# Optimization experiments

Measured on AMD Instinct MI355X. Metric: run time of the kernel, lower is better.

The kernel has to match this reference:

```python
import jax, jax.numpy as jnp
import numpy as np

B, H, S, D = 2, 16, 2048, 64
MASK_P = 0.1  # sparse random mask; avoids all-heads-masked NaN under softmax(dim=1)


def setup_inputs() -> dict:
    key = jax.random.key(0)
    kq, kk, kv, km = jax.random.split(key, 4)
    Q = jax.random.normal(kq, (B, H, S, D), dtype=jnp.float32)
    K = jax.random.normal(kk, (B, H, S, D), dtype=jnp.float32)
    V = jax.random.normal(kv, (B, H, S, D), dtype=jnp.float32)
    mask_bool = jax.random.uniform(km, (B, H, S, S)) < MASK_P
    return {"Q": Q, "K": K, "V": V, "mask_bool": mask_bool, "head_dim": D}


def reference(Q, K, V, mask_bool, head_dim):
    scale = jnp.sqrt(jnp.asarray(head_dim, dtype=Q.dtype))
    # scores: [B, H, Sq, Sk]
    scores = jnp.einsum("bhqd,bhkd->bhqk", Q, K) / scale
    scores = jnp.where(mask_bool, -jnp.inf, scores)
    # NOTE: source uses torch.softmax(..., dim=1) -> normalize over HEADS axis.
    attention_weight = jax.nn.softmax(scores, axis=1)
    # dropout module treated as identity (eval mode)
    context = jnp.einsum("bhqk,bhkd->bhqd", attention_weight, V)
    # transpose(1, 2) -> [B, Sq, H, D]
    return jnp.transpose(context, (0, 2, 1, 3))
```

## Files before the change

### kernel.cpp

```cpp
#include <hip/hip_runtime.h>
#include <stdint.h>
#include <math.h>

#define BB 2
#define HH 16
#define SS 2048
#define DD 64
#define QE  ((size_t)BB * HH * SS * DD)
#define PME ((size_t)BB * SS * SS)

#define WROW 36

typedef __attribute__((ext_vector_type(8))) short short8;
typedef __attribute__((ext_vector_type(4))) float float4v;

__device__ __forceinline__ float bflo(unsigned int u){ return __uint_as_float(u << 16); }
__device__ __forceinline__ float bfhi(unsigned int u){ return __uint_as_float(u & 0xffff0000u); }
__device__ __forceinline__ unsigned short f2bf(float f){
  unsigned int u = __float_as_uint(f);
  u += 0x7fffu + ((u >> 16) & 1u);
  return (unsigned short)(u >> 16);
}
__device__ __forceinline__ unsigned int pk2(float lo, float hi){
  return ((unsigned int)f2bf(hi) << 16) | (unsigned int)f2bf(lo);
}

__global__ void detect_mask_mode(const unsigned int* __restrict__ mw, int* __restrict__ mode_out){
  __shared__ int a32, af, a64;
  const int t = threadIdx.x;
  if (t == 0){ a32 = 1; af = 1; a64 = 1; }
  __syncthreads();
  int ok32 = 1, okf = 1, ok64 = 1;
  for (int idx = t; idx < 4096; idx += 256){
    const unsigned int w = mw[idx];
    if (w > 1u) ok32 = 0;
    if (w != 0u && w != 0x3F800000u) okf = 0;
    if ((idx & 1) ? (w != 0u) : (w > 1u)) ok64 = 0;
  }
  if (!ok32) atomicAnd(&a32, 0);
  if (!okf)  atomicAnd(&af, 0);
  if (!ok64) atomicAnd(&a64, 0);
  __syncthreads();
  if (t == 0){
    int mode;
    if (a64)      mode = 3;
    else if (a32) mode = 0;
    else if (af)  mode = 2;
    else          mode = 1;
    *mode_out = mode;
  }
}

__global__ __launch_bounds__(256) void pack_mask_kernel(
    const void* __restrict__ mask, const int* __restrict__ modep,
    unsigned short* __restrict__ pm)
{
  const int mode = *modep;
  const size_t tid  = (size_t)blockIdx.x * 256 + threadIdx.x;
  const size_t base = tid * 8;
  const size_t bq   = base >> 11;
  const int    k0   = (int)(base & (SS - 1));
  const size_t b    = bq >> 11;
  const size_t q    = bq & (SS - 1);

  unsigned short outv[8] = {0,0,0,0,0,0,0,0};

  if (mode == 0 || mode == 2){
    const unsigned int* p = (const unsigned int*)mask;
    #pragma unroll
    for (int h = 0; h < HH; ++h){
      const size_t e = ((b * HH + h) * SS + q) * SS + k0;
      const uint4 a = *(const uint4*)(p + e);
      const uint4 c = *(const uint4*)(p + e + 4);
      const unsigned short bit = (unsigned short)(1u << h);
      if (a.x) outv[0] |= bit;  if (a.y) outv[1] |= bit;
      if (a.z) outv[2] |= bit;  if (a.w) outv[3] |= bit;
      if (c.x) outv[4] |= bit;  if (c.y) outv[5] |= bit;
      if (c.z) outv[6] |= bit;  if (c.w) outv[7] |= bit;
    }
  } else if (mode == 1){
    const unsigned char* p = (const unsigned char*)mask;
    #pragma unroll
    for (int h = 0; h < HH; ++h){
      const size_t e = ((b * HH + h) * SS + q) * SS + k0;
      uint2 a = *(const uint2*)(p + e);
      const unsigned short bit = (unsigned short)(1u << h);
      #pragma unroll
      for (int j = 0; j < 4; ++j){
        if ((a.x >> (8*j)) & 0xffu) outv[j]     |= bit;
        if ((a.y >> (8*j)) & 0xffu) outv[4 + j] |= bit;
      }
    }
  } else {
    const unsigned int* p = (const unsigned int*)mask;
    #pragma unroll
    for (int h = 0; h < HH; ++h){
      const size_t e = (((b * HH + h) * SS + q) * SS + k0) * 2;
      const unsigned short bit = (unsigned short)(1u << h);
      #pragma unroll
      for (int j = 0; j < 4; ++j){
        const uint4 a = *(const uint4*)(p + e + j * 4);
        if (a.x) outv[j * 2]     |= bit;
        if (a.z) outv[j * 2 + 1] |= bit;
      }
    }
  }

  uint4 w;
  w.x = (unsigned int)outv[0] | ((unsigned int)outv[1] << 16);
  w.y = (unsigned int)outv[2] | ((unsigned int)outv[3] << 16);
  w.z = (unsigned int)outv[4] | ((unsigned int)outv[5] << 16);
  w.w = (unsigned int)outv[6] | ((unsigned int)outv[7] << 16);
  *(uint4*)(pm + base) = w;
}

__global__ void conv_bf16_kernel(const float* __restrict__ src, unsigned short* __restrict__ dst, float scale){
  const size_t i = ((size_t)blockIdx.x * 256 + threadIdx.x) * 8;
  const float4 a = *(const float4*)(src + i);
  const float4 b = *(const float4*)(src + i + 4);
  uint4 o;
  o.x = pk2(a.x * scale, a.y * scale);
  o.y = pk2(a.z * scale, a.w * scale);
  o.z = pk2(b.x * scale, b.y * scale);
  o.w = pk2(b.z * scale, b.w * scale);
  *(uint4*)(dst + i) = o;
}

__global__ void transp_v_kernel(const float* __restrict__ V, unsigned short* __restrict__ Vt){
  __shared__ unsigned short tile[64][66];
  const int t  = threadIdx.x;
  const int kt = blockIdx.x & 31;
  const int bh = blockIdx.x >> 5;
  {
    const int kr = t >> 2, dc = (t & 3) * 16;
    const float* src = V + ((size_t)bh * SS + (size_t)(kt * 64 + kr)) * DD + dc;
    #pragma unroll
    for (int c = 0; c < 4; ++c){
      const float4 v = *(const float4*)(src + c * 4);
      tile[kr][dc + c * 4 + 0] = f2bf(v.x);
      tile[kr][dc + c * 4 + 1] = f2bf(v.y);
      tile[kr][dc + c * 4 + 2] = f2bf(v.z);
      tile[kr][dc + c * 4 + 3] = f2bf(v.w);
    }
  }
  __syncthreads();
  {
    const int dr = t >> 2, kc = (t & 3) * 16;
    unsigned short* dst = Vt + ((size_t)bh * DD + dr) * SS + kt * 64 + kc;
    unsigned int w[8];
    #pragma unroll
    for (int p = 0; p < 8; ++p){
      w[p] = (unsigned int)tile[kc + 2*p][dr] | ((unsigned int)tile[kc + 2*p + 1][dr] << 16);
    }
    uint4 o0 = { w[0], w[1], w[2], w[3] };
    uint4 o1 = { w[4], w[5], w[6], w[7] };
    *(uint4*)(dst)     = o0;
    *(uint4*)(dst + 8) = o1;
  }
}

__global__ __launch_bounds__(128, 2) void attn_main_kernel(
    const unsigned short* __restrict__ Qb, const unsigned short* __restrict__ Kb,
    const unsigned short* __restrict__ Vt, const unsigned short* __restrict__ pm,
    float* __restrict__ out)
{
  __shared__ unsigned int Wp[2][8 * 16 * WROW];

  const int t = threadIdx.x;
  const int wave = t >> 6, lane = t & 63, quad = lane >> 4, l16 = lane & 15;

  const int L  = blockIdx.x;
  const int kc = L & 3;
  const int b  = (L >> 2) & 1;
  const int q0 = (L >> 3) << 4;

  float4v O[8][4];
  #pragma unroll
  for (int i = 0; i < 8; ++i)
    #pragma unroll
    for (int j = 0; j < 4; ++j) O[i][j] = (float4v){0.f, 0.f, 0.f, 0.f};

  const unsigned short* qbase = Qb + ((size_t)(b * HH) * SS + (size_t)(q0 + l16)) * DD + quad * 8;
  const unsigned short* kbas0 = Kb + ((size_t)(b * HH) * SS + (size_t)(kc * 512 + wave * 16 + l16)) * DD + quad * 8;
  const unsigned short* pmrow = pm + ((size_t)b * SS + (size_t)(q0 + quad * 4)) * SS + (size_t)(kc * 512 + wave * 16 + l16);

  unsigned int m16[4];
  #pragma unroll
  for (int r = 0; r < 4; ++r) m16[r] = (unsigned int)pmrow[(size_t)r * SS];

  #pragma unroll 1
  for (int ks = 0; ks < 16; ++ks){
    const int k0 = kc * 512 + ks * 32;

    unsigned int sp[HH][2];
    const unsigned short* kbase = kbas0 + (size_t)ks * 32 * DD;

    #pragma unroll
    for (int ch = 0; ch < 8; ++ch){
      short8 qa0[2], qa1[2], kb0[2], kb1[2];
      #pragma unroll
      for (int j = 0; j < 2; ++j){
        const int h = ch * 2 + j;
        const unsigned short* qp = qbase + (size_t)h * (SS * DD);
        const unsigned short* kp = kbase + (size_t)h * (SS * DD);
        qa0[j] = *(const short8*)(qp);
        qa1[j] = *(const short8*)(qp + 32);
        kb0[j] = *(const short8*)(kp);
        kb1[j] = *(const short8*)(kp + 32);
      }
      #pragma unroll
      for (int j = 0; j < 2; ++j){
        const int h = ch * 2 + j;
        float4v c = (float4v){0.f, 0.f, 0.f, 0.f};
        c = __builtin_amdgcn_mfma_f32_16x16x32_bf16(qa0[j], kb0[j], c, 0, 0, 0);
        c = __builtin_amdgcn_mfma_f32_16x16x32_bf16(qa1[j], kb1[j], c, 0, 0, 0);
        #pragma unroll
        for (int r = 0; r < 4; ++r) if ((m16[r] >> h) & 1u) c[r] = -INFINITY;
        sp[h][0] = pk2(c[0], c[1]);
        sp[h][1] = pk2(c[2], c[3]);
      }
    }

    if (ks < 15){
      #pragma unroll
      for (int r = 0; r < 4; ++r) m16[r] = (unsigned int)pmrow[(size_t)r * SS + (size_t)(ks + 1) * 32];
    }

    unsigned int* Wc = &Wp[ks & 1][0];
    const int kdx = wave * 16 + l16;
    #pragma unroll
    for (int r = 0; r < 4; ++r){
      const int row = quad * 4 + r;
      float sv[HH];
      float m = -INFINITY;
      #pragma unroll
      for (int h = 0; h < HH; ++h){
        const unsigned int u = sp[h][r >> 1];
        const float f = (r & 1) ? bfhi(u) : bflo(u);
        sv[h] = f;
        m = fmaxf(m, f);
      }
      float sum = 0.f;
      #pragma unroll
      for (int h = 0; h < HH; ++h){
        const float e = (sv[h] != -INFINITY) ? __expf(sv[h] - m) : 0.f;
        sv[h] = e;
        sum += e;
      }
      const float rinv = (sum > 0.f) ? (1.0f / sum) : 0.f;
      #pragma unroll
      for (int hp = 0; hp < 8; ++hp){
        Wc[hp * (16 * WROW) + row * WROW + kdx] = pk2(sv[2 * hp] * rinv, sv[2 * hp + 1] * rinv);
      }
    }
    __syncthreads();

    #pragma unroll
    for (int hp2 = 0; hp2 < 4; ++hp2){
      const int hp = wave * 4 + hp2;
      const unsigned int* wb = &Wc[hp * (16 * WROW) + l16 * WROW + quad * 8];
      const uint4 da = *(const uint4*)(wb);
      const uint4 db = *(const uint4*)(wb + 4);
      const unsigned int d0 = da.x, d1 = da.y, d2 = da.z, d3 = da.w;
      const unsigned int d4 = db.x, d5 = db.y, d6 = db.z, d7 = db.w;
      uint4 ue, uo;
      ue.x = (d0 & 0xffffu) | (d1 << 16);
      ue.y = (d2 & 0xffffu) | (d3 << 16);
      ue.z = (d4 & 0xffffu) | (d5 << 16);
      ue.w = (d6 & 0xffffu) | (d7 << 16);
      uo.x = (d0 >> 16) | (d1 & 0xffff0000u);
      uo.y = (d2 >> 16) | (d3 & 0xffff0000u);
      uo.z = (d4 >> 16) | (d5 & 0xffff0000u);
      uo.w = (d6 >> 16) | (d7 & 0xffff0000u);
      const short8 ae = __builtin_bit_cast(short8, ue);
      const short8 ao = __builtin_bit_cast(short8, uo);

      const unsigned short* ve = Vt + ((size_t)(b * HH + 2 * hp) * DD + l16) * SS + k0 + quad * 8;
      const unsigned short* vo = ve + (size_t)SS * DD;
      #pragma unroll
      for (int dt = 0; dt < 4; ++dt){
        const short8 bve = *(const short8*)(ve + (size_t)dt * 16 * SS);
        const short8 bvo = *(const short8*)(vo + (size_t)dt * 16 * SS);
        O[hp2 * 2 + 0][dt] = __builtin_amdgcn_mfma_f32_16x16x32_bf16(ae, bve, O[hp2 * 2 + 0][dt], 0, 0, 0);
        O[hp2 * 2 + 1][dt] = __builtin_amdgcn_mfma_f32_16x16x32_bf16(ao, bvo, O[hp2 * 2 + 1][dt], 0, 0, 0);
      }
    }
  }

  #pragma unroll
  for (int hh = 0; hh < 8; ++hh){
    const int h = wave * 8 + hh;
    #pragma unroll
    for (int dt = 0; dt < 4; ++dt){
      #pragma unroll
      for (int r = 0; r < 4; ++r){
        float* op = out + (((size_t)b * SS + (size_t)(q0 + quad * 4 + r)) * HH + h) * DD + dt * 16 + l16;
        unsafeAtomicAdd(op, O[hh][dt][r]);
      }
    }
  }
}

extern "C" void kernel_launch(void* const* d_in, const int* in_sizes, int n_in,
                              void* d_out, int out_size, void* d_ws, size_t ws_size,
                              hipStream_t stream)
{
  const float* Q = (const float*)d_in[0];
  const float* K = (const float*)d_in[1];
  const float* V = (const float*)d_in[2];
  const void* mask = d_in[3];

  uintptr_t base = (uintptr_t)d_ws;
  int* mode_ptr       = (int*)base;
  unsigned short* Qb  = (unsigned short*)(base + 64);
  unsigned short* Kb  = Qb + QE;
  unsigned short* Vt  = Kb + QE;
  unsigned short* pmp = Vt + QE;

  detect_mask_mode<<<1, 256, 0, stream>>>((const unsigned int*)mask, mode_ptr);
  pack_mask_kernel<<<(int)(PME / (256 * 8)), 256, 0, stream>>>(mask, mode_ptr, pmp);
  conv_bf16_kernel<<<2048, 256, 0, stream>>>(Q, Qb, 0.125f);
  conv_bf16_kernel<<<2048, 256, 0, stream>>>(K, Kb, 1.0f);
  transp_v_kernel<<<BB * HH * (SS / 64), 256, 0, stream>>>(V, Vt);
  hipMemsetAsync(d_out, 0, (size_t)out_size * sizeof(float), stream);

  attn_main_kernel<<<1024, 128, 0, stream>>>(Qb, Kb, Vt, pmp, (float*)d_out);
}
```

Before: 1.124 ms.

## Split attention kernel into producer score waves and consumer PV waves

The main kernel becomes warp-specialized. Two waves compute QK scores, the mask and the head-axis softmax into double-buffered shared memory, and two waves run the PV MFMAs with register-prefetched V tiles. Q is staged once into shared memory and reused across key steps. The key split per block goes from 4 chunks to 2, with 256-thread blocks and half as many blocks, which cuts the atomic adds on the output. The producer and consumer loops sync through matching __syncthreads calls, and this relies on equal iteration counts in both branches.

```diff
diff --git a/kernel.cpp b/kernel.cpp
--- a/kernel.cpp
+++ b/kernel.cpp
@@ -159,143 +159,175 @@
   }
 }
 
-__global__ __launch_bounds__(128, 2) void attn_main_kernel(
+__global__ __launch_bounds__(256, 2) void attn_main_kernel(
     const unsigned short* __restrict__ Qb, const unsigned short* __restrict__ Kb,
     const unsigned short* __restrict__ Vt, const unsigned short* __restrict__ pm,
     float* __restrict__ out)
 {
-  __shared__ unsigned int Wp[2][8 * 16 * WROW];
+  __shared__ unsigned short Qf[HH * 2 * 512];
+  __shared__ unsigned int  Wp[2][8 * 16 * WROW];
 
   const int t = threadIdx.x;
   const int wave = t >> 6, lane = t & 63, quad = lane >> 4, l16 = lane & 15;
 
   const int L  = blockIdx.x;
-  const int kc = L & 3;
-  const int b  = (L >> 2) & 1;
-  const int q0 = (L >> 3) << 4;
-
-  float4v O[8][4];
+  const int b  = (L >> 1) & 1;
+  const int kc = (L >> 2) & 1;
+  const int q0 = (((L >> 3) << 1) | (L & 1)) * 16;
+
   #pragma unroll
-  for (int i = 0; i < 8; ++i)
-    #pragma unroll
-    for (int j = 0; j < 4; ++j) O[i][j] = (float4v){0.f, 0.f, 0.f, 0.f};
-
-  const unsigned short* qbase = Qb + ((size_t)(b * HH) * SS + (size_t)(q0 + l16)) * DD + quad * 8;
-  const unsigned short* kbas0 = Kb + ((size_t)(b * HH) * SS + (size_t)(kc * 512 + wave * 16 + l16)) * DD + quad * 8;
-  const unsigned short* pmrow = pm + ((size_t)b * SS + (size_t)(q0 + quad * 4)) * SS + (size_t)(kc * 512 + wave * 16 + l16);
-
-  unsigned int m16[4];
-  #pragma unroll
-  for (int r = 0; r < 4; ++r) m16[r] = (unsigned int)pmrow[(size_t)r * SS];
-
-  #pragma unroll 1
-  for (int ks = 0; ks < 16; ++ks){
-    const int k0 = kc * 512 + ks * 32;
-
-    unsigned int sp[HH][2];
-    const unsigned short* kbase = kbas0 + (size_t)ks * 32 * DD;
-
-    #pragma unroll
-    for (int ch = 0; ch < 8; ++ch){
-      short8 qa0[2], qa1[2], kb0[2], kb1[2];
-      #pragma unroll
-      for (int j = 0; j < 2; ++j){
-        const int h = ch * 2 + j;
-        const unsigned short* qp = qbase + (size_t)h * (SS * DD);
-        const unsigned short* kp = kbase + (size_t)h * (SS * DD);
-        qa0[j] = *(const short8*)(qp);
-        qa1[j] = *(const short8*)(qp + 32);
-        kb0[j] = *(const short8*)(kp);
-        kb1[j] = *(const short8*)(kp + 32);
-      }
-      #pragma unroll
-      for (int j = 0; j < 2; ++j){
-        const int h = ch * 2 + j;
-        float4v c = (float4v){0.f, 0.f, 0.f, 0.f};
-        c = __builtin_amdgcn_mfma_f32_16x16x32_bf16(qa0[j], kb0[j], c, 0, 0, 0);
-        c = __builtin_amdgcn_mfma_f32_16x16x32_bf16(qa1[j], kb1[j], c, 0, 0, 0);
-        #pragma unroll
-        for (int r = 0; r < 4; ++r) if ((m16[r] >> h) & 1u) c[r] = -INFINITY;
-        sp[h][0] = pk2(c[0], c[1]);
-        sp[h][1] = pk2(c[2], c[3]);
-      }
-    }
-
-    if (ks < 15){
-      #pragma unroll
-      for (int r = 0; r < 4; ++r) m16[r] = (unsigned int)pmrow[(size_t)r * SS + (size_t)(ks + 1) * 32];
-    }
-
-    unsigned int* Wc = &Wp[ks & 1][0];
-    const int kdx = wave * 16 + l16;
-    #pragma unroll
-    for (int r = 0; r < 4; ++r){
-      const int row = quad * 4 + r;
-      float sv[HH];
-      float m = -INFINITY;
-      #pragma unroll
-      for (int h = 0; h < HH; ++h){
-        const unsigned int u = sp[h][r >> 1];
-        const float f = (r & 1) ? bfhi(u) : bflo(u);
-        sv[h] = f;
-        m = fmaxf(m, f);
-      }
-      float sum = 0.f;
-      #pragma unroll
-      for (int h = 0; h < HH; ++h){
-        const float e = (sv[h] != -INFINITY) ? __expf(sv[h] - m) : 0.f;
-        sv[h] = e;
-        sum += e;
-      }
-      const float rinv = (sum > 0.f) ? (1.0f / sum) : 0.f;
-      #pragma unroll
-      for (int hp = 0; hp < 8; ++hp){
-        Wc[hp * (16 * WROW) + row * WROW + kdx] = pk2(sv[2 * hp] * rinv, sv[2 * hp + 1] * rinv);
-      }
-    }
-    __syncthreads();
-
-    #pragma unroll
-    for (int hp2 = 0; hp2 < 4; ++hp2){
-      const int hp = wave * 4 + hp2;
-      const unsigned int* wb = &Wc[hp * (16 * WROW) + l16 * WROW + quad * 8];
-      const uint4 da = *(const uint4*)(wb);
-      const uint4 db = *(const uint4*)(wb + 4);
-      const unsigned int d0 = da.x, d1 = da.y, d2 = da.z, d3 = da.w;
-      const unsigned int d4 = db.x, d5 = db.y, d6 = db.z, d7 = db.w;
-      uint4 ue, uo;
-      ue.x = (d0 & 0xffffu) | (d1 << 16);
-      ue.y = (d2 & 0xffffu) | (d3 << 16);
-      ue.z = (d4 & 0xffffu) | (d5 << 16);
-      ue.w = (d6 & 0xffffu) | (d7 << 16);
-      uo.x = (d0 >> 16) | (d1 & 0xffff0000u);
-      uo.y = (d2 >> 16) | (d3 & 0xffff0000u);
-      uo.z = (d4 >> 16) | (d5 & 0xffff0000u);
-      uo.w = (d6 >> 16) | (d7 & 0xffff0000u);
-      const short8 ae = __builtin_bit_cast(short8, ue);
-      const short8 ao = __builtin_bit_cast(short8, uo);
-
-      const unsigned short* ve = Vt + ((size_t)(b * HH + 2 * hp) * DD + l16) * SS + k0 + quad * 8;
-      const unsigned short* vo = ve + (size_t)SS * DD;
+  for (int hh = 0; hh < 4; ++hh){
+    const int h = wave * 4 + hh;
+    const unsigned short* qp = Qb + ((size_t)(b * HH + h) * SS + (size_t)(q0 + l16)) * DD + quad * 8;
+    *(short8*)&Qf[(h * 2 + 0) * 512 + lane * 8] = *(const short8*)(qp);
+    *(short8*)&Qf[(h * 2 + 1) * 512 + lane * 8] = *(const short8*)(qp + 32);
+  }
+  __syncthreads();
+
+  if (wave < 2){
+    const int p = wave;
+    const unsigned short* kbas0 = Kb + ((size_t)(b * HH) * SS + (size_t)(kc * 1024 + p * 16 + l16)) * DD + quad * 8;
+    const unsigned short* pmrow = pm + ((size_t)b * SS + (size_t)(q0 + quad * 4)) * SS + (size_t)(kc * 1024 + p * 16 + l16);
+
+    unsigned int m16[4];
+    #pragma unroll
+    for (int r = 0; r < 4; ++r) m16[r] = (unsigned int)pmrow[(size_t)r * SS];
+
+    #pragma unroll 1
+    for (int ks = 0; ks < 32; ++ks){
+      unsigned int sp[HH][2];
+      const unsigned short* kbase = kbas0 + (size_t)ks * 32 * DD;
+
+      #pragma unroll
+      for (int ch = 0; ch < 4; ++ch){
+        short8 kb0[4], kb1[4];
+        #pragma unroll
+        for (int j = 0; j < 4; ++j){
+          const unsigned short* kp = kbase + (size_t)(ch * 4 + j) * (SS * DD);
+          kb0[j] = *(const short8*)(kp);
+          kb1[j] = *(const short8*)(kp + 32);
+        }
+        #pragma unroll
+        for (int j = 0; j < 4; ++j){
+          const int h = ch * 4 + j;
+          const short8 a0 = *(const short8*)&Qf[(h * 2 + 0) * 512 + lane * 8];
+          const short8 a1 = *(const short8*)&Qf[(h * 2 + 1) * 512 + lane * 8];
+          float4v c = (float4v){0.f, 0.f, 0.f, 0.f};
+          c = __builtin_amdgcn_mfma_f32_16x16x32_bf16(a0, kb0[j], c, 0, 0, 0);
+          c = __builtin_amdgcn_mfma_f32_16x16x32_bf16(a1, kb1[j], c, 0, 0, 0);
+          #pragma unroll
+          for (int r = 0; r < 4; ++r) if ((m16[r] >> h) & 1u) c[r] = -INFINITY;
+          sp[h][0] = pk2(c[0], c[1]);
+          sp[h][1] = pk2(c[2], c[3]);
+        }
+      }
+
+      if (ks < 31){
+        #pragma unroll
+        for (int r = 0; r < 4; ++r) m16[r] = (unsigned int)pmrow[(size_t)r * SS + (size_t)(ks + 1) * 32];
+      }
+
+      unsigned int* Wc = &Wp[ks & 1][0];
+      const int kdx = p * 16 + l16;
+      #pragma unroll
+      for (int r = 0; r < 4; ++r){
+        const int row = quad * 4 + r;
+        float sv[HH];
+        float m = -INFINITY;
+        #pragma unroll
+        for (int h = 0; h < HH; ++h){
+          const unsigned int u = sp[h][r >> 1];
+          const float f = (r & 1) ? bfhi(u) : bflo(u);
+          sv[h] = f;
+          m = fmaxf(m, f);
+        }
+        float sum = 0.f;
+        #pragma unroll
+        for (int h = 0; h < HH; ++h){
+          const float e = (sv[h] != -INFINITY) ? __expf(sv[h] - m) : 0.f;
+          sv[h] = e;
+          sum += e;
+        }
+        const float rinv = (sum > 0.f) ? (1.0f / sum) : 0.f;
+        #pragma unroll
+        for (int hp = 0; hp < 8; ++hp){
+          Wc[hp * (16 * WROW) + row * WROW + kdx] = pk2(sv[2 * hp] * rinv, sv[2 * hp + 1] * rinv);
+        }
+      }
+      __syncthreads();
+    }
+  } else {
+    const int c = wave - 2;
+    float4v O[8][4];
+    #pragma unroll
+    for (int i = 0; i < 8; ++i)
+      #pragma unroll
+      for (int j = 0; j < 4; ++j) O[i][j] = (float4v){0.f, 0.f, 0.f, 0.f};
+
+    #pragma unroll 1
+    for (int ks = 0; ks < 32; ++ks){
+      const int k0 = kc * 1024 + ks * 32;
+
+      short8 vb[2][8];
+      {
+        const int hp = c * 4;
+        const unsigned short* ve = Vt + ((size_t)(b * HH + 2 * hp) * DD + l16) * SS + k0 + quad * 8;
+        const unsigned short* vo = ve + (size_t)SS * DD;
+        #pragma unroll
+        for (int dt = 0; dt < 4; ++dt){
+          vb[0][dt]     = *(const short8*)(ve + (size_t)dt * 16 * SS);
+          vb[0][4 + dt] = *(const short8*)(vo + (size_t)dt * 16 * SS);
+        }
+      }
+      __syncthreads();
+
+      const unsigned int* Wc = &Wp[ks & 1][0];
+      #pragma unroll
+      for (int hp2 = 0; hp2 < 4; ++hp2){
+        const int cur = hp2 & 1;
+        if (hp2 < 3){
+          const int hpn = c * 4 + hp2 + 1;
+          const unsigned short* ve = Vt + ((size_t)(b * HH + 2 * hpn) * DD + l16) * SS + k0 + quad * 8;
+          const unsigned short* vo = ve + (size_t)SS * DD;
+          #pragma unroll
+          for (int dt = 0; dt < 4; ++dt){
+            vb[cur ^ 1][dt]     = *(const short8*)(ve + (size_t)dt * 16 * SS);
+            vb[cur ^ 1][4 + dt] = *(const short8*)(vo + (size_t)dt * 16 * SS);
+          }
+        }
+        const int hp = c * 4 + hp2;
+        const unsigned int* wb = &Wc[hp * (16 * WROW) + l16 * WROW + quad * 8];
+        const uint4 da = *(const uint4*)(wb);
+        const uint4 db = *(const uint4*)(wb + 4);
+        uint4 ue, uo;
+        ue.x = (da.x & 0xffffu) | (da.y << 16);
+        ue.y = (da.z & 0xffffu) | (da.w << 16);
+        ue.z = (db.x & 0xffffu) | (db.y << 16);
+        ue.w = (db.z & 0xffffu) | (db.w << 16);
+        uo.x = (da.x >> 16) | (da.y & 0xffff0000u);
+        uo.y = (da.z >> 16) | (da.w & 0xffff0000u);
+        uo.z = (db.x >> 16) | (db.y & 0xffff0000u);
+        uo.w = (db.z >> 16) | (db.w & 0xffff0000u);
+        const short8 ae = __builtin_bit_cast(short8, ue);
+        const short8 ao = __builtin_bit_cast(short8, uo);
+        #pragma unroll
+        for (int dt = 0; dt < 4; ++dt){
+          O[hp2 * 2 + 0][dt] = __builtin_amdgcn_mfma_f32_16x16x32_bf16(ae, vb[cur][dt],     O[hp2 * 2 + 0][dt], 0, 0, 0);
+          O[hp2 * 2 + 1][dt] = __builtin_amdgcn_mfma_f32_16x16x32_bf16(ao, vb[cur][4 + dt], O[hp2 * 2 + 1][dt], 0, 0, 0);
+        }
+      }
+    }
+
+    #pragma unroll
+    for (int j = 0; j < 8; ++j){
+      const int h = c * 8 + j;
       #pragma unroll
       for (int dt = 0; dt < 4; ++dt){
-        const short8 bve = *(const short8*)(ve + (size_t)dt * 16 * SS);
-        const short8 bvo = *(const short8*)(vo + (size_t)dt * 16 * SS);
-        O[hp2 * 2 + 0][dt] = __builtin_amdgcn_mfma_f32_16x16x32_bf16(ae, bve, O[hp2 * 2 + 0][dt], 0, 0, 0);
-        O[hp2 * 2 + 1][dt] = __builtin_amdgcn_mfma_f32_16x16x32_bf16(ao, bvo, O[hp2 * 2 + 1][dt], 0, 0, 0);
-      }
-    }
-  }
-
-  #pragma unroll
-  for (int hh = 0; hh < 8; ++hh){
-    const int h = wave * 8 + hh;
-    #pragma unroll
-    for (int dt = 0; dt < 4; ++dt){
-      #pragma unroll
-      for (int r = 0; r < 4; ++r){
-        float* op = out + (((size_t)b * SS + (size_t)(q0 + quad * 4 + r)) * HH + h) * DD + dt * 16 + l16;
-        unsafeAtomicAdd(op, O[hh][dt][r]);
+        #pragma unroll
+        for (int r = 0; r < 4; ++r){
+          float* op = out + (((size_t)b * SS + (size_t)(q0 + quad * 4 + r)) * HH + h) * DD + dt * 16 + l16;
+          unsafeAtomicAdd(op, O[j][dt][r]);
+        }
       }
     }
   }
@@ -324,5 +356,5 @@
   transp_v_kernel<<<BB * HH * (SS / 64), 256, 0, stream>>>(V, Vt);
   hipMemsetAsync(d_out, 0, (size_t)out_size * sizeof(float), stream);
 
-  attn_main_kernel<<<1024, 128, 0, stream>>>(Qb, Kb, Vt, pmp, (float*)d_out);
-}
+  attn_main_kernel<<<512, 256, 0, stream>>>(Qb, Kb, Vt, pmp, (float*)d_out);
+}
```

New measurement: 1.017 ms. 1.11x faster.
